# Optimization experiments

Measured on AMD Instinct MI355X. Metric: run time of the kernel, lower is better.

## Reference

```python
import jax, jax.numpy as jnp
import numpy as np
import math
from functools import partial

PHI = (1.0 + math.sqrt(5.0)) / 2.0
RES = 4096            # lut_resolution
D = 128               # d_model
TWO_PI = 2.0 * math.pi


def _lookup_sin_cos(theta, sin_t, cos_t):
    # Quantize angle to LUT index (assumed round-to-nearest, wrap mod 2*pi)
    idx = jnp.mod(jnp.round(theta * (RES / TWO_PI)).astype(jnp.int32), RES)
    return sin_t[idx], cos_t[idx]


def setup_inputs() -> dict:
    key = jax.random.key(0)
    ks = jax.random.split(key, 7)
    B, S, V, L, N = 8, 256, 50257, 2, 256
    return {
        "input_ids": jax.random.randint(ks[0], (B, S), 0, V),
        "emb": jax.random.normal(ks[1], (V, 2 * D), dtype=jnp.float32) * 0.01,
        "layer_W": jax.random.normal(ks[2], (L, N, D), dtype=jnp.float32) * 0.02,
        "layer_b": jax.random.normal(ks[3], (L, N), dtype=jnp.float32) * 0.02,
        "layer_Wr": jax.random.normal(ks[4], (L, D, N), dtype=jnp.float32) * 0.02,
        "layer_Wi": jax.random.normal(ks[5], (L, D, N), dtype=jnp.float32) * 0.02,
        "out_w": jax.random.normal(ks[6], (V, D), dtype=jnp.float32) * 0.02,
    }


def reference(input_ids, emb, layer_W, layer_b, layer_Wr, layer_Wi, out_w):
    B, S = input_ids.shape
    L = layer_W.shape[0]
    angles = jnp.arange(RES, dtype=jnp.float32) * (TWO_PI / RES)
    sin_t, cos_t = jnp.sin(angles), jnp.cos(angles)

    e = emb[input_ids]                       # (B, S, 2D) embedding gather
    w_emb, b_emb = e[..., :D], e[..., D:]

    def step(carry, xs):
        h_real, h_imag = carry
        w_t, b_t, t = xs                     # w_t,b_t: (B,D); t: scalar
        t_phi = t * PHI
        # euler_transform: theta = (h_r+h_i)/(1+|w|) + b + t*phi
        theta = (h_real + h_imag) / (1.0 + jnp.abs(w_t)) + b_t + t_phi
        h_imag, h_real = _lookup_sin_cos(theta, sin_t, cos_t)
        x = h_real + h_imag                  # (B, D)
        for i in range(L):                   # small fixed layer loop
            th = x @ layer_W[i].T + layer_b[i] + t_phi   # (B, N)
            sn, cs = _lookup_sin_cos(th, sin_t, cos_t)
            o = cs @ layer_Wr[i].T + sn @ layer_Wi[i].T  # (B, D)
            x = x + jax.nn.silu(o)
        logits = x @ out_w.T                 # (B, V)
        return (h_real, h_imag), logits

    ts = jnp.arange(S, dtype=jnp.float32)    # t_start = 0
    h0 = (jnp.zeros((B, D), jnp.float32), jnp.zeros((B, D), jnp.float32))
    xs = (jnp.swapaxes(w_emb, 0, 1), jnp.swapaxes(b_emb, 0, 1), ts)
    (h_real, h_imag), logits = jax.lax.scan(step, h0, xs)
    return jnp.swapaxes(logits, 0, 1), h_real, h_imag  # (B,S,V), (B,D), (B,D)
```

## Files before the change

### kernel.cpp

```cpp
#include <hip/hip_runtime.h>

#define BATCH 8
#define SEQ   256
#define VOC   50257
#define DIM   128
#define NH    256
#define LOGITS_ELEMS 102926336ULL

constexpr float PHI_F   = 1.61803398874989485f;
constexpr float SCALE_F = (float)(4096.0 / 6.283185307179586);
constexpr float STEP_F  = (float)(6.283185307179586 / 4096.0);

__device__ __forceinline__ unsigned short f2bf(float f) {
    unsigned int u = __float_as_uint(f);
    u = (u + 0x7fffu + ((u >> 16) & 1u)) >> 16;
    return (unsigned short)u;
}

__global__ __launch_bounds__(256) void prep_kernel(
        const float* __restrict__ emb,
        const int*   __restrict__ ids,
        const float* __restrict__ W,
        const float* __restrict__ Wr,
        const float* __restrict__ Wi,
        const float* __restrict__ outw,
        unsigned short* __restrict__ outw_bf,
        float* __restrict__ wt,
        float* __restrict__ wrt,
        float* __restrict__ wit,
        float* __restrict__ X0,
        float* __restrict__ out) {
    int bid = blockIdx.x;
    int tid = threadIdx.x;
    if (bid < 8) {
        __shared__ int ids_s[256];
        ids_s[tid] = ids[bid * 256 + tid];
        __syncthreads();
        if (tid >= 128) return;
        const int b = bid, d = tid;
        float wA[16], bA[16], wB[16], bB[16];
        #pragma unroll
        for (int u = 0; u < 16; ++u) {
            const float* e = emb + (size_t)ids_s[u] * 256 + d;
            wA[u] = e[0]; bA[u] = e[128];
        }
        float hr = 0.0f, hi = 0.0f;
        float* X0p = X0 + b * 128 + d;
        for (int t0 = 0; t0 < 256; t0 += 32) {
            #pragma unroll
            for (int u = 0; u < 16; ++u) {
                const float* e = emb + (size_t)ids_s[t0 + 16 + u] * 256 + d;
                wB[u] = e[0]; bB[u] = e[128];
            }
            #pragma unroll
            for (int u = 0; u < 16; ++u) {
                int t = t0 + u;
                float tphi = (float)t * PHI_F;
                float th = (hr + hi) / (1.0f + fabsf(wA[u])) + bA[u] + tphi;
                int idx = ((int)rintf(th * SCALE_F)) & 4095;
                float ang = (float)idx * STEP_F;
                hi = __sinf(ang); hr = __cosf(ang);
                X0p[t * 1024] = hr + hi;
            }
            if (t0 + 32 < 256) {
                #pragma unroll
                for (int u = 0; u < 16; ++u) {
                    const float* e = emb + (size_t)ids_s[t0 + 32 + u] * 256 + d;
                    wA[u] = e[0]; bA[u] = e[128];
                }
            }
            #pragma unroll
            for (int u = 0; u < 16; ++u) {
                int t = t0 + 16 + u;
                float tphi = (float)t * PHI_F;
                float th = (hr + hi) / (1.0f + fabsf(wB[u])) + bB[u] + tphi;
                int idx = ((int)rintf(th * SCALE_F)) & 4095;
                float ang = (float)idx * STEP_F;
                hi = __sinf(ang); hr = __cosf(ang);
                X0p[t * 1024] = hr + hi;
            }
        }
        out[LOGITS_ELEMS + b * 128 + d] = hr;
        out[LOGITS_ELEMS + 1024 + b * 128 + d] = hi;
    } else if (bid < 6291) {
        int i4 = (bid - 8) * 256 + tid;
        if (i4 < (VOC * DIM) / 4) {
            float4 v = ((const float4*)outw)[i4];
            unsigned int lo = ((unsigned)f2bf(v.y) << 16) | f2bf(v.x);
            unsigned int hi = ((unsigned)f2bf(v.w) << 16) | f2bf(v.z);
            ((uint2*)outw_bf)[i4] = make_uint2(lo, hi);
        }
    } else {
        int e = (bid - 6291) * 256 + tid;
        int tns = e >> 16;
        int r = e & 65535;
        int i = r >> 15, rem = r & 32767;
        if (tns == 0) {
            int dd = rem >> 8, n = rem & 255;
            wt[r] = W[(i * 256 + n) * 128 + dd];
        } else if (tns == 1) {
            int n = rem >> 7, dd = rem & 127;
            wrt[r] = Wr[(i * 128 + dd) * 256 + n];
        } else {
            int n = rem >> 7, dd = rem & 127;
            wit[r] = Wi[(i * 128 + dd) * 256 + n];
        }
    }
}

__global__ __launch_bounds__(1024) void layers_kernel(
        const float* __restrict__ X0,
        const float* __restrict__ wt,
        const float* __restrict__ wrt,
        const float* __restrict__ wit,
        const float* __restrict__ lb,
        unsigned short* __restrict__ X2bf) {
    __shared__ __align__(16) float xs[128 * 12];
    __shared__ __align__(16) float csh[256 * 12];
    __shared__ __align__(16) float snh[256 * 12];
    __shared__ __align__(16) float red[7168];
    int tid = threadIdx.x, t = blockIdx.x;
    float tphi = (float)t * PHI_F;
    if (tid < 256) {
        float4 v = ((const float4*)(X0 + t * 1024))[tid];
        int r = tid >> 5, d0 = (tid & 31) << 2;
        xs[(d0 + 0) * 12 + r] = v.x;
        xs[(d0 + 1) * 12 + r] = v.y;
        xs[(d0 + 2) * 12 + r] = v.z;
        xs[(d0 + 3) * 12 + r] = v.w;
    }
    __syncthreads();
    int n  = tid & 255, q1 = tid >> 8;
    int d2 = tid & 127, q2 = tid >> 7;
    for (int i = 0; i < 2; ++i) {
        const float* wti = wt + i * 32768;
        float acc[8] = {0,0,0,0,0,0,0,0};
        int dlo = q1 << 5;
        #pragma unroll 4
        for (int dd = 0; dd < 32; ++dd) {
            int d = dlo + dd;
            float wv = wti[d * 256 + n];
            float4 x0 = *(const float4*)&xs[d * 12];
            float4 x1 = *(const float4*)&xs[d * 12 + 4];
            acc[0] += x0.x * wv; acc[1] += x0.y * wv;
            acc[2] += x0.z * wv; acc[3] += x0.w * wv;
            acc[4] += x1.x * wv; acc[5] += x1.y * wv;
            acc[6] += x1.z * wv; acc[7] += x1.w * wv;
        }
        if (q1) {
            float* p = &red[(q1 - 1) * 2048 + n * 8];
            *(float4*)p       = make_float4(acc[0], acc[1], acc[2], acc[3]);
            *(float4*)(p + 4) = make_float4(acc[4], acc[5], acc[6], acc[7]);
        }
        __syncthreads();
        if (!q1) {
            #pragma unroll
            for (int qq = 0; qq < 3; ++qq) {
                const float* p = &red[qq * 2048 + n * 8];
                float4 p0 = *(const float4*)p;
                float4 p1 = *(const float4*)(p + 4);
                acc[0] += p0.x; acc[1] += p0.y; acc[2] += p0.z; acc[3] += p0.w;
                acc[4] += p1.x; acc[5] += p1.y; acc[6] += p1.z; acc[7] += p1.w;
            }
            float bv = lb[i * 256 + n];
            float cs[8], sn[8];
            #pragma unroll
            for (int r = 0; r < 8; ++r) {
                float th = acc[r] + bv + tphi;
                int idx = ((int)rintf(th * SCALE_F)) & 4095;
                float ang = (float)idx * STEP_F;
                cs[r] = __cosf(ang);
                sn[r] = __sinf(ang);
            }
            *(float4*)&csh[n * 12]     = make_float4(cs[0], cs[1], cs[2], cs[3]);
            *(float4*)&csh[n * 12 + 4] = make_float4(cs[4], cs[5], cs[6], cs[7]);
            *(float4*)&snh[n * 12]     = make_float4(sn[0], sn[1], sn[2], sn[3]);
            *(float4*)&snh[n * 12 + 4] = make_float4(sn[4], sn[5], sn[6], sn[7]);
        }
        __syncthreads();
        const float* wri = wrt + i * 32768;
        const float* wii = wit + i * 32768;
        float a2[8] = {0,0,0,0,0,0,0,0};
        int nlo = q2 << 5;
        #pragma unroll 2
        for (int k = 0; k < 32; ++k) {
            int nidx = nlo + k;
            float rv = wri[nidx * 128 + d2];
            float iv = wii[nidx * 128 + d2];
            float4 c0 = *(const float4*)&csh[nidx * 12];
            float4 c1 = *(const float4*)&csh[nidx * 12 + 4];
            float4 s0 = *(const float4*)&snh[nidx * 12];
            float4 s1 = *(const float4*)&snh[nidx * 12 + 4];
            a2[0] += c0.x * rv + s0.x * iv;
            a2[1] += c0.y * rv + s0.y * iv;
            a2[2] += c0.z * rv + s0.z * iv;
            a2[3] += c0.w * rv + s0.w * iv;
            a2[4] += c1.x * rv + s1.x * iv;
            a2[5] += c1.y * rv + s1.y * iv;
            a2[6] += c1.z * rv + s1.z * iv;
            a2[7] += c1.w * rv + s1.w * iv;
        }
        if (q2) {
            float* p = &red[(q2 - 1) * 1024 + d2 * 8];
            *(float4*)p       = make_float4(a2[0], a2[1], a2[2], a2[3]);
            *(float4*)(p + 4) = make_float4(a2[4], a2[5], a2[6], a2[7]);
        }
        __syncthreads();
        if (!q2) {
            #pragma unroll
            for (int qq = 0; qq < 7; ++qq) {
                const float* p = &red[qq * 1024 + d2 * 8];
                float4 p0 = *(const float4*)p;
                float4 p1 = *(const float4*)(p + 4);
                a2[0] += p0.x; a2[1] += p0.y; a2[2] += p0.z; a2[3] += p0.w;
                a2[4] += p1.x; a2[5] += p1.y; a2[6] += p1.z; a2[7] += p1.w;
            }
            float4 xv0 = *(const float4*)&xs[d2 * 12];
            float4 xv1 = *(const float4*)&xs[d2 * 12 + 4];
            float xv[8] = {xv0.x, xv0.y, xv0.z, xv0.w, xv1.x, xv1.y, xv1.z, xv1.w};
            #pragma unroll
            for (int r = 0; r < 8; ++r) {
                float o = a2[r];
                float sg = 1.0f / (1.0f + __expf(-o));
                xv[r] += o * sg;
            }
            *(float4*)&xs[d2 * 12]     = make_float4(xv[0], xv[1], xv[2], xv[3]);
            *(float4*)&xs[d2 * 12 + 4] = make_float4(xv[4], xv[5], xv[6], xv[7]);
        }
        __syncthreads();
    }
    if (tid < 256) {
        int r = tid >> 5, d0 = (tid & 31) << 2;
        float v0 = xs[(d0 + 0) * 12 + r];
        float v1 = xs[(d0 + 1) * 12 + r];
        float v2 = xs[(d0 + 2) * 12 + r];
        float v3 = xs[(d0 + 3) * 12 + r];
        unsigned int lo = ((unsigned)f2bf(v1) << 16) | f2bf(v0);
        unsigned int hi = ((unsigned)f2bf(v3) << 16) | f2bf(v2);
        ((uint2*)(X2bf + t * 1024))[tid] = make_uint2(lo, hi);
    }
}

typedef short bhalf8 __attribute__((ext_vector_type(8)));
typedef float fx4    __attribute__((ext_vector_type(4)));

__global__ __launch_bounds__(512) void gemm_kernel(
        const unsigned short* __restrict__ X2bf,
        const unsigned short* __restrict__ outw_bf,
        float* __restrict__ out) {
    __shared__ __align__(16) unsigned short Ash[16384];
    int tid = threadIdx.x;
    int mt = blockIdx.x & 15;
    int vt = blockIdx.x >> 4;
    for (int s = tid; s < 2048; s += 512) {
        int blk = s >> 6, ln = s & 63;
        int msub = blk >> 2, ks = blk & 3;
        int row = mt * 128 + msub * 16 + (ln & 15);
        int kel = ks * 32 + ((ln >> 4) << 3);
        ((int4*)Ash)[s] = *(const int4*)(X2bf + row * 128 + kel);
    }
    __syncthreads();
    int lane = tid & 63, wave = tid >> 6;
    int wm = wave >> 2;
    int wn = wave & 3;
    int ln15 = lane & 15, lq = lane >> 4;
    int vb = vt * 256 + wn * 64;
    fx4 acc[4][4] = {};
    const bhalf8* Af = (const bhalf8*)Ash;
    #pragma unroll
    for (int ks = 0; ks < 4; ++ks) {
        bhalf8 xf[4];
        #pragma unroll
        for (int jm = 0; jm < 4; ++jm)
            xf[jm] = Af[((wm * 4 + jm) * 4 + ks) * 64 + lane];
        bhalf8 wf[4];
        #pragma unroll
        for (int iv = 0; iv < 4; ++iv) {
            int v = vb + iv * 16 + ln15;
            bhalf8 z = {};
            wf[iv] = z;
            if (v < VOC)
                wf[iv] = *(const bhalf8*)(outw_bf + v * 128 + ks * 32 + lq * 8);
        }
        #pragma unroll
        for (int iv = 0; iv < 4; ++iv) {
            #pragma unroll
            for (int jm = 0; jm < 4; ++jm)
                acc[iv][jm] = __builtin_amdgcn_mfma_f32_16x16x32_bf16(
                    wf[iv], xf[jm], acc[iv][jm], 0, 0, 0);
        }
    }
    #pragma unroll
    for (int jm = 0; jm < 4; ++jm) {
        int m = mt * 128 + wm * 64 + jm * 16 + ln15;
        float* rp = out + (size_t)((m & 7) * SEQ + (m >> 3)) * VOC;
        #pragma unroll
        for (int iv = 0; iv < 4; ++iv) {
            int v4 = vb + iv * 16 + lq * 4;
            fx4 a = acc[iv][jm];
            if (v4 + 3 < VOC) {
                *(float4*)(rp + v4) = make_float4(a[0], a[1], a[2], a[3]);
            } else {
                #pragma unroll
                for (int e = 0; e < 4; ++e)
                    if (v4 + e < VOC) rp[v4 + e] = a[e];
            }
        }
    }
}

extern "C" void kernel_launch(void* const* d_in, const int* in_sizes, int n_in,
                              void* d_out, int out_size, void* d_ws, size_t ws_size,
                              hipStream_t stream) {
    const int*   ids  = (const int*)d_in[0];
    const float* emb  = (const float*)d_in[1];
    const float* W    = (const float*)d_in[2];
    const float* lb   = (const float*)d_in[3];
    const float* Wr   = (const float*)d_in[4];
    const float* Wi   = (const float*)d_in[5];
    const float* outw = (const float*)d_in[6];
    float* out = (float*)d_out;
    char* ws = (char*)d_ws;

    unsigned short* outw_bf = (unsigned short*)ws;
    float* wt    = (float*)(ws + 12865792);
    float* wrt   = wt + 65536;
    float* wit   = wrt + 65536;
    float* X0    = wit + 65536;
    unsigned short* X2bf = (unsigned short*)(X0 + 262144);

    prep_kernel<<<7059, 256, 0, stream>>>(emb, ids, W, Wr, Wi, outw,
                                          outw_bf, wt, wrt, wit, X0, out);
    layers_kernel<<<256, 1024, 0, stream>>>(X0, wt, wrt, wit, lb, X2bf);
    gemm_kernel<<<197 * 16, 512, 0, stream>>>(X2bf, outw_bf, out);
}
```

Before: 591.3 us.

## Overlap out_w bf16 conversion with layers kernel and remap GEMM block order

Moves the out_w fp32-to-bf16 conversion out of the prep kernel and into extra blocks of the layers kernel. The intent is for the conversion to fill CUs left idle by the 256 recurrent-layer blocks instead of delaying the serial recurrence in prep. The GEMM gets a block-index swizzle over 8 groups, and a FULL template specialisation drops the vocab bounds checks for every tile except the last. The extra blocks make layers_kernel reserve its large shared-memory footprint even though they use none, which may limit co-residency.

After: 626.4 us. 5.9% more time.

```diff
diff --git a/kernel.cpp b/kernel.cpp
--- a/kernel.cpp
+++ b/kernel.cpp
@@ -17,14 +17,12 @@
     return (unsigned short)u;
 }
 
-__global__ __launch_bounds__(256) void prep_kernel(
+__global__ __launch_bounds__(256) void prep1_kernel(
         const float* __restrict__ emb,
         const int*   __restrict__ ids,
         const float* __restrict__ W,
         const float* __restrict__ Wr,
         const float* __restrict__ Wi,
-        const float* __restrict__ outw,
-        unsigned short* __restrict__ outw_bf,
         float* __restrict__ wt,
         float* __restrict__ wrt,
         float* __restrict__ wit,
@@ -82,16 +80,8 @@
         }
         out[LOGITS_ELEMS + b * 128 + d] = hr;
         out[LOGITS_ELEMS + 1024 + b * 128 + d] = hi;
-    } else if (bid < 6291) {
-        int i4 = (bid - 8) * 256 + tid;
-        if (i4 < (VOC * DIM) / 4) {
-            float4 v = ((const float4*)outw)[i4];
-            unsigned int lo = ((unsigned)f2bf(v.y) << 16) | f2bf(v.x);
-            unsigned int hi = ((unsigned)f2bf(v.w) << 16) | f2bf(v.z);
-            ((uint2*)outw_bf)[i4] = make_uint2(lo, hi);
-        }
     } else {
-        int e = (bid - 6291) * 256 + tid;
+        int e = (bid - 8) * 256 + tid;
         int tns = e >> 16;
         int r = e & 65535;
         int i = r >> 15, rem = r & 32767;
@@ -114,12 +104,24 @@
         const float* __restrict__ wrt,
         const float* __restrict__ wit,
         const float* __restrict__ lb,
-        unsigned short* __restrict__ X2bf) {
+        unsigned short* __restrict__ X2bf,
+        const float* __restrict__ outw,
+        unsigned short* __restrict__ outw_bf) {
+    int tid = threadIdx.x, t = blockIdx.x;
+    if (t >= 256) {
+        int i4 = (t - 256) * 1024 + tid;
+        if (i4 < (VOC * DIM) / 4) {
+            float4 v = ((const float4*)outw)[i4];
+            unsigned int lo = ((unsigned)f2bf(v.y) << 16) | f2bf(v.x);
+            unsigned int hi = ((unsigned)f2bf(v.w) << 16) | f2bf(v.z);
+            ((uint2*)outw_bf)[i4] = make_uint2(lo, hi);
+        }
+        return;
+    }
     __shared__ __align__(16) float xs[128 * 12];
     __shared__ __align__(16) float csh[256 * 12];
     __shared__ __align__(16) float snh[256 * 12];
     __shared__ __align__(16) float red[7168];
-    int tid = threadIdx.x, t = blockIdx.x;
     float tphi = (float)t * PHI_F;
     if (tid < 256) {
         float4 v = ((const float4*)(X0 + t * 1024))[tid];
@@ -244,25 +246,12 @@
 typedef short bhalf8 __attribute__((ext_vector_type(8)));
 typedef float fx4    __attribute__((ext_vector_type(4)));
 
-__global__ __launch_bounds__(512) void gemm_kernel(
-        const unsigned short* __restrict__ X2bf,
+template <bool FULL>
+__device__ __forceinline__ void gemm_body(
+        const unsigned short* __restrict__ Ash,
         const unsigned short* __restrict__ outw_bf,
-        float* __restrict__ out) {
-    __shared__ __align__(16) unsigned short Ash[16384];
-    int tid = threadIdx.x;
-    int mt = blockIdx.x & 15;
-    int vt = blockIdx.x >> 4;
-    for (int s = tid; s < 2048; s += 512) {
-        int blk = s >> 6, ln = s & 63;
-        int msub = blk >> 2, ks = blk & 3;
-        int row = mt * 128 + msub * 16 + (ln & 15);
-        int kel = ks * 32 + ((ln >> 4) << 3);
-        ((int4*)Ash)[s] = *(const int4*)(X2bf + row * 128 + kel);
-    }
-    __syncthreads();
-    int lane = tid & 63, wave = tid >> 6;
-    int wm = wave >> 2;
-    int wn = wave & 3;
+        float* __restrict__ out,
+        int mt, int vt, int lane, int wm, int wn) {
     int ln15 = lane & 15, lq = lane >> 4;
     int vb = vt * 256 + wn * 64;
     fx4 acc[4][4] = {};
@@ -277,10 +266,14 @@
         #pragma unroll
         for (int iv = 0; iv < 4; ++iv) {
             int v = vb + iv * 16 + ln15;
-            bhalf8 z = {};
-            wf[iv] = z;
-            if (v < VOC)
-                wf[iv] = *(const bhalf8*)(outw_bf + v * 128 + ks * 32 + lq * 8);
+            if (FULL) {
+                wf[iv] = *(const bhalf8*)(outw_bf + (size_t)v * 128 + ks * 32 + lq * 8);
+            } else {
+                bhalf8 z = {};
+                wf[iv] = z;
+                if (v < VOC)
+                    wf[iv] = *(const bhalf8*)(outw_bf + (size_t)v * 128 + ks * 32 + lq * 8);
+            }
         }
         #pragma unroll
         for (int iv = 0; iv < 4; ++iv) {
@@ -298,7 +291,9 @@
         for (int iv = 0; iv < 4; ++iv) {
             int v4 = vb + iv * 16 + lq * 4;
             fx4 a = acc[iv][jm];
-            if (v4 + 3 < VOC) {
+            if (FULL) {
+                *(float4*)(rp + v4) = make_float4(a[0], a[1], a[2], a[3]);
+            } else if (v4 + 3 < VOC) {
                 *(float4*)(rp + v4) = make_float4(a[0], a[1], a[2], a[3]);
             } else {
                 #pragma unroll
@@ -307,6 +302,33 @@
             }
         }
     }
+}
+
+__global__ __launch_bounds__(512) void gemm_kernel(
+        const unsigned short* __restrict__ X2bf,
+        const unsigned short* __restrict__ outw_bf,
+        float* __restrict__ out) {
+    __shared__ __align__(16) unsigned short Ash[16384];
+    int tid = threadIdx.x;
+    int bid = blockIdx.x;
+    int b2 = (bid & 7) * 394 + (bid >> 3);
+    int mt = b2 & 15;
+    int vt = b2 >> 4;
+    for (int s = tid; s < 2048; s += 512) {
+        int blk = s >> 6, ln = s & 63;
+        int msub = blk >> 2, ks = blk & 3;
+        int row = mt * 128 + msub * 16 + (ln & 15);
+        int kel = ks * 32 + ((ln >> 4) << 3);
+        ((int4*)Ash)[s] = *(const int4*)(X2bf + row * 128 + kel);
+    }
+    __syncthreads();
+    int lane = tid & 63, wave = tid >> 6;
+    int wm = wave >> 2;
+    int wn = wave & 3;
+    if (vt < 196)
+        gemm_body<true>(Ash, outw_bf, out, mt, vt, lane, wm, wn);
+    else
+        gemm_body<false>(Ash, outw_bf, out, mt, vt, lane, wm, wn);
 }
 
 extern "C" void kernel_launch(void* const* d_in, const int* in_sizes, int n_in,
@@ -329,8 +351,9 @@
     float* X0    = wit + 65536;
     unsigned short* X2bf = (unsigned short*)(X0 + 262144);
 
-    prep_kernel<<<7059, 256, 0, stream>>>(emb, ids, W, Wr, Wi, outw,
-                                          outw_bf, wt, wrt, wit, X0, out);
-    layers_kernel<<<256, 1024, 0, stream>>>(X0, wt, wrt, wit, lb, X2bf);
-    gemm_kernel<<<197 * 16, 512, 0, stream>>>(X2bf, outw_bf, out);
-}
+    prep1_kernel<<<776, 256, 0, stream>>>(emb, ids, W, Wr, Wi,
+                                          wt, wrt, wit, X0, out);
+    layers_kernel<<<1827, 1024, 0, stream>>>(X0, wt, wrt, wit, lb, X2bf,
+                                             outw, outw_bf);
+    gemm_kernel<<<3152, 512, 0, stream>>>(X2bf, outw_bf, out);
+}
```
